# Optimization experiments

Hardware: AMD Instinct MI355X
Metric: run time of the kernel (lower is better)

## Reference

```python
import jax, jax.numpy as jnp
import numpy as np

B, S, H = 2, 2048, 1024
E, K, I = 8, 2, 512
NSH = 2
IS = I * NSH           # shared-expert intermediate = moe_inter * n_shared_experts
NUM_TASKS = 3
TEMP = 1.0             # router_temperature_init (eval: no annealing, no noise)


def setup_inputs() -> dict:
    key = jax.random.key(0)
    ks = jax.random.split(key, 11)
    s_h = 1.0 / np.sqrt(H).astype(np.float32)
    s_i = 1.0 / np.sqrt(I).astype(np.float32)
    s_is = 1.0 / np.sqrt(IS).astype(np.float32)
    return {
        "hidden_states": jax.random.normal(ks[0], (B, S, H), jnp.float32),
        "task_id": 1,
        "gate_w": jax.random.normal(ks[1], (E, H), jnp.float32) * s_h,
        "task_emb": jax.random.normal(ks[2], (NUM_TASKS, H), jnp.float32) * 0.02,
        "We_gate": jax.random.normal(ks[3], (E, H, I), jnp.float32) * s_h,
        "We_up": jax.random.normal(ks[4], (E, H, I), jnp.float32) * s_h,
        "We_down": jax.random.normal(ks[5], (E, I, H), jnp.float32) * s_i,
        "Ws_gate": jax.random.normal(ks[6], (H, IS), jnp.float32) * s_h,
        "Ws_up": jax.random.normal(ks[7], (H, IS), jnp.float32) * s_h,
        "Ws_down": jax.random.normal(ks[8], (IS, H), jnp.float32) * s_is,
        "Wc": jax.random.normal(ks[9], (H, 2), jnp.float32) * s_h,
    }


def _gelu(x):
    return jax.nn.gelu(x, approximate=False)  # matches torch F.gelu default (erf)


def reference(hidden_states, task_id, gate_w, task_emb, We_gate, We_up, We_down,
              Ws_gate, Ws_up, Ws_down, Wc):
    b, s, h = hidden_states.shape
    flat = hidden_states.reshape(-1, h)            # [T, H]
    T = flat.shape[0]

    # ---- NoisyTopKGating (eval: no gumbel noise, no dropout, no aux loss) ----
    gate_in = flat + task_emb[task_id]             # task-conditioned router input
    logits = (gate_in @ gate_w.T) / TEMP           # [T, E]
    scores = jax.nn.softmax(logits, axis=-1)
    topk_w, topk_idx = jax.lax.top_k(scores, K)    # [T, K]
    topk_w = topk_w / (topk_w.sum(-1, keepdims=True) + 1e-20)  # norm_topk_prob

    # dense combine weights [T, E]: zero except the top-k routed experts
    w_dense = jnp.zeros((T, E), scores.dtype).at[
        jnp.arange(T)[:, None], topk_idx].set(topk_w)

    # ---- routed experts: gated MLP per expert, weighted scatter-combine ----
    g = _gelu(jnp.einsum('td,edi->eti', flat, We_gate))   # [E, T, I]
    u = jnp.einsum('td,edi->eti', flat, We_up)            # [E, T, I]
    local = jnp.einsum('eti,te,eid->td', g * u, w_dense, We_down)
    local = local.reshape(b, s, h)

    # ---- shared expert (wider gated MLP over all tokens) ----
    shared = (_gelu(hidden_states @ Ws_gate) * (hidden_states @ Ws_up)) @ Ws_down

    # ---- combination gate: softmax over (local, shared) ----
    alpha = jax.nn.softmax(hidden_states @ Wc, axis=-1)   # [B, S, 2]
    return alpha[..., 0:1] * local + alpha[..., 1:2] * shared
```

## Files before the change

kernel.cpp:

```cpp
#include <hip/hip_runtime.h>
#include <hip/hip_bf16.h>


typedef short  s16x8 __attribute__((ext_vector_type(8)));
typedef __bf16 bf16x8 __attribute__((ext_vector_type(8)));
typedef float  f32x4 __attribute__((ext_vector_type(4)));

__device__ __forceinline__ float b2f(ushort u) {
  union { unsigned int i; float f; } v; v.i = ((unsigned int)u) << 16; return v.f;
}
__device__ __forceinline__ ushort f2b(float f) {
  union { float f; unsigned int i; } v; v.f = f;
  unsigned int r = v.i + 0x7fffu + ((v.i >> 16) & 1u);
  return (ushort)(r >> 16);
}
__device__ __forceinline__ f32x4 mfma_bf16(s16x8 a, s16x8 b, f32x4 c) {
  return __builtin_amdgcn_mfma_f32_16x16x32_bf16(
      __builtin_bit_cast(bf16x8, a), __builtin_bit_cast(bf16x8, b), c, 0, 0, 0);
}
__device__ __forceinline__ void gll16(const ushort* g, const ushort* l) {
  __builtin_amdgcn_global_load_lds(
      (const __attribute__((address_space(1))) unsigned int*)g,
      (__attribute__((address_space(3))) unsigned int*)l, 16, 0, 0);
}

__global__ __launch_bounds__(256) void transpose_all_k(
    const float* __restrict__ Weg, const float* __restrict__ Weu,
    const float* __restrict__ Wed, const float* __restrict__ Wsg,
    const float* __restrict__ Wsu, const float* __restrict__ Wsd,
    ushort* __restrict__ GT, ushort* __restrict__ UT, ushort* __restrict__ DT)
{
  const int z = blockIdx.z;
  const float* src; ushort* dst; int srcLd, dstLd, nx, ny;
  if (z < 8)       { src = Weg + (size_t)z * 512 * 1024;      dst = GT + (size_t)z * 512 * 1024; srcLd = 512;  dstLd = 1024; nx = 16; ny = 32; }
  else if (z < 16) { src = Weu + (size_t)(z - 8) * 512 * 1024; dst = UT + (size_t)(z - 8) * 512 * 1024; srcLd = 512; dstLd = 1024; nx = 16; ny = 32; }
  else if (z < 24) { src = Wed + (size_t)(z - 16) * 512 * 1024; dst = DT + (size_t)(z - 16) * 512; srcLd = 1024; dstLd = 5120; nx = 32; ny = 16; }
  else if (z == 24){ src = Wsg; dst = GT + 4096 * 1024; srcLd = 1024; dstLd = 1024; nx = 32; ny = 32; }
  else if (z == 25){ src = Wsu; dst = UT + 4096 * 1024; srcLd = 1024; dstLd = 1024; nx = 32; ny = 32; }
  else             { src = Wsd; dst = DT + 4096;        srcLd = 1024; dstLd = 5120; nx = 32; ny = 32; }
  if ((int)blockIdx.x >= nx || (int)blockIdx.y >= ny) return;

  __shared__ float tile[32][33];
  const int c0 = blockIdx.x * 32, r0 = blockIdx.y * 32;
  const int tx = threadIdx.x & 31, ty = threadIdx.x >> 5;
#pragma unroll
  for (int j = 0; j < 4; ++j)
    tile[ty + j * 8][tx] = src[(size_t)(r0 + ty + j * 8) * srcLd + c0 + tx];
  __syncthreads();
#pragma unroll
  for (int j = 0; j < 4; ++j)
    dst[(size_t)(c0 + ty + j * 8) * dstLd + r0 + tx] = f2b(tile[tx][ty + j * 8]);
}

__global__ __launch_bounds__(256) void router_k(
    const float* __restrict__ X, const float* __restrict__ Gw,
    const float* __restrict__ Temb, const int* __restrict__ task_id,
    const float* __restrict__ Wc, float* __restrict__ scales,
    int* __restrict__ topk, ushort* __restrict__ Xb)
{
  const int wid = threadIdx.x >> 6, lane = threadIdx.x & 63;
  const int t = blockIdx.x * 4 + wid;
  const float* xr = X + t * 1024;
  const float* er = Temb + task_id[0] * 1024;

  float x[16], xe[16];
#pragma unroll
  for (int c = 0; c < 4; ++c) {
    float4 v = *(const float4*)&xr[c * 256 + lane * 4];
    float4 e = *(const float4*)&er[c * 256 + lane * 4];
    x[c * 4 + 0] = v.x; x[c * 4 + 1] = v.y; x[c * 4 + 2] = v.z; x[c * 4 + 3] = v.w;
    xe[c * 4 + 0] = v.x + e.x; xe[c * 4 + 1] = v.y + e.y;
    xe[c * 4 + 2] = v.z + e.z; xe[c * 4 + 3] = v.w + e.w;
  }
#pragma unroll
  for (int c = 0; c < 4; ++c) {
    ushort4 o;
    o.x = f2b(x[c * 4 + 0]); o.y = f2b(x[c * 4 + 1]);
    o.z = f2b(x[c * 4 + 2]); o.w = f2b(x[c * 4 + 3]);
    *(ushort4*)&Xb[t * 1024 + c * 256 + lane * 4] = o;
  }
  float logit[8];
#pragma unroll
  for (int e = 0; e < 8; ++e) {
    float p = 0.f;
#pragma unroll
    for (int c = 0; c < 4; ++c) {
      float4 g = *(const float4*)&Gw[e * 1024 + c * 256 + lane * 4];
      p += xe[c * 4] * g.x + xe[c * 4 + 1] * g.y + xe[c * 4 + 2] * g.z + xe[c * 4 + 3] * g.w;
    }
#pragma unroll
    for (int off = 32; off; off >>= 1) p += __shfl_xor(p, off);
    logit[e] = p;
  }
  float m = logit[0];
#pragma unroll
  for (int e = 1; e < 8; ++e) m = fmaxf(m, logit[e]);
  float pr[8], s = 0.f;
#pragma unroll
  for (int e = 0; e < 8; ++e) { pr[e] = expf(logit[e] - m); s += pr[e]; }
  float inv = 1.f / s;
#pragma unroll
  for (int e = 0; e < 8; ++e) pr[e] *= inv;
  int i1 = 0; float m1 = pr[0];
#pragma unroll
  for (int e = 1; e < 8; ++e) if (pr[e] > m1) { m1 = pr[e]; i1 = e; }
  int i2 = -1; float m2 = -1.f;
#pragma unroll
  for (int e = 0; e < 8; ++e) if (e != i1 && pr[e] > m2) { m2 = pr[e]; i2 = e; }
  float dn = 1.f / (m1 + m2 + 1e-20f);
  float w1 = m1 * dn, w2 = m2 * dn;

  float a0 = 0.f, a1 = 0.f;
#pragma unroll
  for (int c = 0; c < 4; ++c)
#pragma unroll
    for (int j = 0; j < 4; ++j) {
      int h = c * 256 + lane * 4 + j;
      a0 += x[c * 4 + j] * Wc[h * 2];
      a1 += x[c * 4 + j] * Wc[h * 2 + 1];
    }
#pragma unroll
  for (int off = 32; off; off >>= 1) {
    a0 += __shfl_xor(a0, off); a1 += __shfl_xor(a1, off);
  }
  float am = fmaxf(a0, a1);
  float ea0 = expf(a0 - am), ea1 = expf(a1 - am);
  float al0 = ea0 / (ea0 + ea1), al1 = ea1 / (ea0 + ea1);

  if (lane == 0) {
    scales[t * 4 + 0] = al0 * w1;
    scales[t * 4 + 1] = al0 * w2;
    scales[t * 4 + 2] = al1;
    topk[t * 2 + 0] = i1;
    topk[t * 2 + 1] = i2;
  }
}

__global__ __launch_bounds__(256) void indexbuild_k(
    const int* __restrict__ topk, const float* __restrict__ scales,
    int* __restrict__ tokmap, int* __restrict__ tokrows,
    float* __restrict__ rowscale, int* __restrict__ meta)
{
  __shared__ int cnt[8], cnt2[8], base[8];
  const int tid = threadIdx.x;
  if (tid < 8) { cnt[tid] = 0; cnt2[tid] = 0; }
  __syncthreads();
  for (int t = tid; t < 4096; t += 256) {
    atomicAdd(&cnt[topk[t * 2]], 1);
    atomicAdd(&cnt[topk[t * 2 + 1]], 1);
  }
  __syncthreads();
  if (tid == 0) {
    int nb = 0;
    for (int e = 0; e < 8; ++e) {
      base[e] = nb * 128;
      int blocks = (cnt[e] + 127) >> 7;
      for (int j = 0; j < blocks; ++j) meta[nb + j] = e;
      nb += blocks;
    }
    meta[127] = nb;
  }
  __syncthreads();
  for (int t = tid; t < 4096; t += 256) {
#pragma unroll
    for (int r = 0; r < 2; ++r) {
      int e = topk[t * 2 + r];
      int slot = atomicAdd(&cnt2[e], 1);
      int row = base[e] + slot;
      tokmap[row] = t;
      rowscale[row] = scales[t * 4 + r];
      tokrows[t * 2 + r] = row;
    }
  }
  __syncthreads();
  for (int e = 0; e < 8; ++e) {
    int c = cnt[e], R = ((c + 127) >> 7) << 7;
    for (int j = c + tid; j < R; j += 256) {
      tokmap[base[e] + j] = 0;
      rowscale[base[e] + j] = 0.f;
    }
  }
}

__global__ __launch_bounds__(256) void gemm1_k(
    const ushort* __restrict__ Xb, const ushort* __restrict__ GT,
    const ushort* __restrict__ UT, const float* __restrict__ scales,
    const int* __restrict__ tokmap, const float* __restrict__ rowscale,
    const int* __restrict__ meta, ushort* __restrict__ Bg,
    ushort* __restrict__ Bs)
{
  __shared__ __align__(16) ushort lA[128 * 64];
  __shared__ __align__(16) ushort lG[64 * 64];
  __shared__ __align__(16) ushort lU[64 * 64];
  const int x = blockIdx.x, y = blockIdx.y;
  const bool routed = y < 72;
  if (routed && (x >= 8 || y >= meta[127])) return;

  const int tid = threadIdx.x, wid = tid >> 6, lane = tid & 63;
  const int col0 = x * 64;
  const int row0 = routed ? y * 128 : (y - 72) * 128;
  const int colG = routed ? (meta[y] * 512 + col0) : (4096 + col0);
  const int wr = (wid >> 1) * 64, wc = (wid & 1) * 32;
  ushort* __restrict__ Out = routed ? Bg : Bs;
  const int outLd = routed ? 512 : 1024;

  int aOff[4], gOff[2], ldsA[4], ldsG[2];
#pragma unroll
  for (int i = 0; i < 4; ++i) {
    int q = (i * 4 + wid) * 64 + lane;
    int r = q >> 3, c = q & 7, lc = c ^ (r & 7);
    int arow = routed ? tokmap[row0 + r] : (row0 + r);
    aOff[i] = arow * 1024 + lc * 8;
    ldsA[i] = (i * 4 + wid) * 512;
  }
#pragma unroll
  for (int i = 0; i < 2; ++i) {
    int q = (i * 4 + wid) * 64 + lane;
    int r = q >> 3, c = q & 7, lc = c ^ (r & 7);
    gOff[i] = (colG + r) * 1024 + lc * 8;
    ldsG[i] = (i * 4 + wid) * 512;
  }

  f32x4 accG[4][2] = {};
  f32x4 accU[4][2] = {};
  for (int k0 = 0; k0 < 1024; k0 += 64) {
    if (k0) __syncthreads();
#pragma unroll
    for (int i = 0; i < 4; ++i) gll16(Xb + aOff[i] + k0, lA + ldsA[i]);
#pragma unroll
    for (int i = 0; i < 2; ++i) gll16(GT + gOff[i] + k0, lG + ldsG[i]);
#pragma unroll
    for (int i = 0; i < 2; ++i) gll16(UT + gOff[i] + k0, lU + ldsG[i]);
    __syncthreads();
#pragma unroll
    for (int kc = 0; kc < 2; ++kc) {
      const int clog = kc * 4 + (lane >> 4);
      s16x8 af[4], gf[2], uf[2];
#pragma unroll
      for (int fr = 0; fr < 4; ++fr) {
        int rl = wr + fr * 16 + (lane & 15);
        af[fr] = *(const s16x8*)&lA[rl * 64 + ((clog ^ (rl & 7)) << 3)];
      }
#pragma unroll
      for (int cf = 0; cf < 2; ++cf) {
        int cl = wc + cf * 16 + (lane & 15);
        int off = cl * 64 + ((clog ^ (cl & 7)) << 3);
        gf[cf] = *(const s16x8*)&lG[off];
        uf[cf] = *(const s16x8*)&lU[off];
      }
#pragma unroll
      for (int fr = 0; fr < 4; ++fr)
#pragma unroll
        for (int cf = 0; cf < 2; ++cf) {
          accG[fr][cf] = mfma_bf16(af[fr], gf[cf], accG[fr][cf]);
          accU[fr][cf] = mfma_bf16(af[fr], uf[cf], accU[fr][cf]);
        }
    }
  }
#pragma unroll
  for (int fr = 0; fr < 4; ++fr)
#pragma unroll
    for (int r = 0; r < 4; ++r) {
      const int row = row0 + wr + fr * 16 + ((lane >> 4) << 2) + r;
      const float sc = routed ? rowscale[row] : scales[row * 4 + 2];
#pragma unroll
      for (int cf = 0; cf < 2; ++cf) {
        const int col = col0 + wc + cf * 16 + (lane & 15);
        float g = accG[fr][cf][r];
        float u = accU[fr][cf][r];
        float a = 0.5f * g * (1.0f + erff(g * 0.70710678118654752f));
        Out[(size_t)row * outLd + col] = f2b(a * u * sc);
      }
    }
}

template<int ROUTED>
__global__ __launch_bounds__(256) void gemm2_k(
    const ushort* __restrict__ A, const ushort* __restrict__ DT,
    const int* __restrict__ meta, const int* __restrict__ tokrows,
    const ushort* __restrict__ Rrows, ushort* __restrict__ OutB,
    float* __restrict__ OutF)
{
  __shared__ __align__(16) ushort lA[128 * 64];
  __shared__ __align__(16) ushort lB[128 * 64];
  int e = 0;
  if (ROUTED) {
    if ((int)blockIdx.y >= meta[127]) return;
    e = meta[blockIdx.y];
  }
  const int K = ROUTED ? 512 : 1024;
  const int bBase = ROUTED ? e * 512 : 4096;
  const int tid = threadIdx.x, wid = tid >> 6, lane = tid & 63;
  const int col0 = blockIdx.x * 128, row0 = blockIdx.y * 128;
  const int wr = (wid >> 1) * 64, wc = (wid & 1) * 64;

  int aOff[4], bOff[4], lds[4];
#pragma unroll
  for (int i = 0; i < 4; ++i) {
    int q = (i * 4 + wid) * 64 + lane;
    int r = q >> 3, c = q & 7, lc = c ^ (r & 7);
    aOff[i] = (row0 + r) * K + lc * 8;
    bOff[i] = (col0 + r) * 5120 + bBase + lc * 8;
    lds[i]  = (i * 4 + wid) * 512;
  }
  f32x4 acc[4][4] = {};
  for (int k0 = 0; k0 < K; k0 += 64) {
    if (k0) __syncthreads();
#pragma unroll
    for (int i = 0; i < 4; ++i) gll16(A + aOff[i] + k0, lA + lds[i]);
#pragma unroll
    for (int i = 0; i < 4; ++i) gll16(DT + bOff[i] + k0, lB + lds[i]);
    __syncthreads();
#pragma unroll
    for (int kc = 0; kc < 2; ++kc) {
      const int clog = kc * 4 + (lane >> 4);
      s16x8 af[4], bf[4];
#pragma unroll
      for (int fr = 0; fr < 4; ++fr) {
        int rl = wr + fr * 16 + (lane & 15);
        af[fr] = *(const s16x8*)&lA[rl * 64 + ((clog ^ (rl & 7)) << 3)];
      }
#pragma unroll
      for (int cf = 0; cf < 4; ++cf) {
        int cl = wc + cf * 16 + (lane & 15);
        bf[cf] = *(const s16x8*)&lB[cl * 64 + ((clog ^ (cl & 7)) << 3)];
      }
#pragma unroll
      for (int fr = 0; fr < 4; ++fr)
#pragma unroll
        for (int cf = 0; cf < 4; ++cf)
          acc[fr][cf] = mfma_bf16(af[fr], bf[cf], acc[fr][cf]);
    }
  }
#pragma unroll
  for (int fr = 0; fr < 4; ++fr)
#pragma unroll
    for (int r = 0; r < 4; ++r) {
      const int row = row0 + wr + fr * 16 + ((lane >> 4) << 2) + r;
      if (ROUTED) {
#pragma unroll
        for (int cf = 0; cf < 4; ++cf) {
          const int col = col0 + wc + cf * 16 + (lane & 15);
          OutB[row * 1024 + col] = f2b(acc[fr][cf][r]);
        }
      } else {
        const int r0 = tokrows[row * 2], r1 = tokrows[row * 2 + 1];
#pragma unroll
        for (int cf = 0; cf < 4; ++cf) {
          const int col = col0 + wc + cf * 16 + (lane & 15);
          float v = acc[fr][cf][r]
                  + b2f(Rrows[r0 * 1024 + col]) + b2f(Rrows[r1 * 1024 + col]);
          OutF[row * 1024 + col] = v;
        }
      }
    }
}

extern "C" void kernel_launch(void* const* d_in, const int* in_sizes, int n_in,
                              void* d_out, int out_size, void* d_ws, size_t ws_size,
                              hipStream_t stream) {
  const float* X    = (const float*)d_in[0];
  const int*   task = (const int*)  d_in[1];
  const float* Gw   = (const float*)d_in[2];
  const float* Temb = (const float*)d_in[3];
  const float* Weg  = (const float*)d_in[4];
  const float* Weu  = (const float*)d_in[5];
  const float* Wed  = (const float*)d_in[6];
  const float* Wsg  = (const float*)d_in[7];
  const float* Wsu  = (const float*)d_in[8];
  const float* Wsd  = (const float*)d_in[9];
  const float* Wc   = (const float*)d_in[10];

  char* ws = (char*)d_ws;
  float*  scales   = (float*)(ws + 0x00000);
  int*    topk     = (int*)  (ws + 0x10000);
  int*    tokmap   = (int*)  (ws + 0x18000);
  int*    tokrows  = (int*)  (ws + 0x22000);
  float*  rowscale = (float*)(ws + 0x2A000);
  int*    meta     = (int*)  (ws + 0x34000);
  ushort* Xb       = (ushort*)(ws + 0x40000);
  ushort* GT       = Xb + 4096 * 1024;
  ushort* UT       = GT + 5120 * 1024;
  ushort* DT       = UT + 5120 * 1024;
  ushort* Bg       = DT + 1024 * 5120;
  ushort* Bs       = Bg + 9216 * 512;
  ushort* out_r    = Bs + 4096 * 1024;

  transpose_all_k<<<dim3(32, 32, 27), 256, 0, stream>>>(
      Weg, Weu, Wed, Wsg, Wsu, Wsd, GT, UT, DT);

  router_k<<<1024, 256, 0, stream>>>(X, Gw, Temb, task, Wc, scales, topk, Xb);
  indexbuild_k<<<1, 256, 0, stream>>>(topk, scales, tokmap, tokrows, rowscale, meta);

  gemm1_k<<<dim3(16, 104), 256, 0, stream>>>(Xb, GT, UT, scales, tokmap, rowscale, meta, Bg, Bs);

  gemm2_k<1><<<dim3(8, 72), 256, 0, stream>>>(Bg, DT, meta, tokrows, (const ushort*)nullptr, out_r, (float*)nullptr);
  gemm2_k<0><<<dim3(8, 32), 256, 0, stream>>>(Bs, DT, meta, tokrows, out_r, (ushort*)nullptr, (float*)d_out);
}
```

Before: 176.7 us.

## Double-buffer LDS in both GEMM kernels and split transpose into exact grids

Both GEMM kernels move from a single LDS buffer to two ping-ponged buffers. The next K-tile is loaded with global_load_lds while the current one feeds the MFMAs, using explicit vmcnt waits and barriers, so load latency overlaps compute. The weight transpose is split into three launches whose grids match each matrix shape, which avoids launching blocks that exit at once. Doubling LDS use (64KB per block in gemm2) may lower occupancy, and the hand-written waitcnt counts must match the number of outstanding loads per stage.

```diff
diff --git a/kernel.cpp b/kernel.cpp
--- a/kernel.cpp
+++ b/kernel.cpp
@@ -24,22 +24,26 @@
       (__attribute__((address_space(3))) unsigned int*)l, 16, 0, 0);
 }
 
-__global__ __launch_bounds__(256) void transpose_all_k(
-    const float* __restrict__ Weg, const float* __restrict__ Weu,
-    const float* __restrict__ Wed, const float* __restrict__ Wsg,
-    const float* __restrict__ Wsu, const float* __restrict__ Wsd,
-    ushort* __restrict__ GT, ushort* __restrict__ UT, ushort* __restrict__ DT)
+template<int MODE>
+__global__ __launch_bounds__(256) void transpose_k(
+    const float* __restrict__ S0, const float* __restrict__ S1,
+    const float* __restrict__ S2, ushort* __restrict__ D0,
+    ushort* __restrict__ D1, ushort* __restrict__ D2)
 {
   const int z = blockIdx.z;
-  const float* src; ushort* dst; int srcLd, dstLd, nx, ny;
-  if (z < 8)       { src = Weg + (size_t)z * 512 * 1024;      dst = GT + (size_t)z * 512 * 1024; srcLd = 512;  dstLd = 1024; nx = 16; ny = 32; }
-  else if (z < 16) { src = Weu + (size_t)(z - 8) * 512 * 1024; dst = UT + (size_t)(z - 8) * 512 * 1024; srcLd = 512; dstLd = 1024; nx = 16; ny = 32; }
-  else if (z < 24) { src = Wed + (size_t)(z - 16) * 512 * 1024; dst = DT + (size_t)(z - 16) * 512; srcLd = 1024; dstLd = 5120; nx = 32; ny = 16; }
-  else if (z == 24){ src = Wsg; dst = GT + 4096 * 1024; srcLd = 1024; dstLd = 1024; nx = 32; ny = 32; }
-  else if (z == 25){ src = Wsu; dst = UT + 4096 * 1024; srcLd = 1024; dstLd = 1024; nx = 32; ny = 32; }
-  else             { src = Wsd; dst = DT + 4096;        srcLd = 1024; dstLd = 5120; nx = 32; ny = 32; }
-  if ((int)blockIdx.x >= nx || (int)blockIdx.y >= ny) return;
-
+  const float* src; ushort* dst; int srcLd, dstLd;
+  if (MODE == 0) {
+    src = (z < 8 ? S0 + (size_t)z * 512 * 1024 : S1 + (size_t)(z - 8) * 512 * 1024);
+    dst = (z < 8 ? D0 + (size_t)z * 512 * 1024 : D1 + (size_t)(z - 8) * 512 * 1024);
+    srcLd = 512; dstLd = 1024;
+  } else if (MODE == 1) {
+    src = S0 + (size_t)z * 512 * 1024; dst = D0 + (size_t)z * 512;
+    srcLd = 1024; dstLd = 5120;
+  } else {
+    src = (z == 0 ? S0 : z == 1 ? S1 : S2);
+    dst = (z == 0 ? D0 : z == 1 ? D1 : D2);
+    srcLd = 1024; dstLd = (z == 2 ? 5120 : 1024);
+  }
   __shared__ float tile[32][33];
   const int c0 = blockIdx.x * 32, r0 = blockIdx.y * 32;
   const int tx = threadIdx.x & 31, ty = threadIdx.x >> 5;
@@ -189,9 +193,9 @@
     const int* __restrict__ meta, ushort* __restrict__ Bg,
     ushort* __restrict__ Bs)
 {
-  __shared__ __align__(16) ushort lA[128 * 64];
-  __shared__ __align__(16) ushort lG[64 * 64];
-  __shared__ __align__(16) ushort lU[64 * 64];
+  __shared__ __align__(16) ushort lA[2][128 * 64];
+  __shared__ __align__(16) ushort lG[2][64 * 64];
+  __shared__ __align__(16) ushort lU[2][64 * 64];
   const int x = blockIdx.x, y = blockIdx.y;
   const bool routed = y < 72;
   if (routed && (x >= 8 || y >= meta[127])) return;
@@ -223,15 +227,16 @@
 
   f32x4 accG[4][2] = {};
   f32x4 accU[4][2] = {};
-  for (int k0 = 0; k0 < 1024; k0 += 64) {
-    if (k0) __syncthreads();
-#pragma unroll
-    for (int i = 0; i < 4; ++i) gll16(Xb + aOff[i] + k0, lA + ldsA[i]);
-#pragma unroll
-    for (int i = 0; i < 2; ++i) gll16(GT + gOff[i] + k0, lG + ldsG[i]);
-#pragma unroll
-    for (int i = 0; i < 2; ++i) gll16(UT + gOff[i] + k0, lU + ldsG[i]);
-    __syncthreads();
+
+  auto stage = [&](ushort* A_, ushort* G_, ushort* U_, int k0) {
+#pragma unroll
+    for (int i = 0; i < 4; ++i) gll16(Xb + aOff[i] + k0, A_ + ldsA[i]);
+#pragma unroll
+    for (int i = 0; i < 2; ++i) gll16(GT + gOff[i] + k0, G_ + ldsG[i]);
+#pragma unroll
+    for (int i = 0; i < 2; ++i) gll16(UT + gOff[i] + k0, U_ + ldsG[i]);
+  };
+  auto compute = [&](const ushort* A_, const ushort* G_, const ushort* U_) {
 #pragma unroll
     for (int kc = 0; kc < 2; ++kc) {
       const int clog = kc * 4 + (lane >> 4);
@@ -239,14 +244,14 @@
 #pragma unroll
       for (int fr = 0; fr < 4; ++fr) {
         int rl = wr + fr * 16 + (lane & 15);
-        af[fr] = *(const s16x8*)&lA[rl * 64 + ((clog ^ (rl & 7)) << 3)];
+        af[fr] = *(const s16x8*)&A_[rl * 64 + ((clog ^ (rl & 7)) << 3)];
       }
 #pragma unroll
       for (int cf = 0; cf < 2; ++cf) {
         int cl = wc + cf * 16 + (lane & 15);
         int off = cl * 64 + ((clog ^ (cl & 7)) << 3);
-        gf[cf] = *(const s16x8*)&lG[off];
-        uf[cf] = *(const s16x8*)&lU[off];
+        gf[cf] = *(const s16x8*)&G_[off];
+        uf[cf] = *(const s16x8*)&U_[off];
       }
 #pragma unroll
       for (int fr = 0; fr < 4; ++fr)
@@ -256,7 +261,28 @@
           accU[fr][cf] = mfma_bf16(af[fr], uf[cf], accU[fr][cf]);
         }
     }
-  }
+  };
+
+  stage(lA[0], lG[0], lU[0], 0);
+  for (int k0 = 0; k0 < 1024; k0 += 128) {
+    stage(lA[1], lG[1], lU[1], k0 + 64);
+    asm volatile("s_waitcnt vmcnt(8)" ::: "memory");
+    __builtin_amdgcn_s_barrier();
+    compute(lA[0], lG[0], lU[0]);
+    asm volatile("s_waitcnt lgkmcnt(0)" ::: "memory");
+    __builtin_amdgcn_s_barrier();
+    if (k0 + 128 < 1024) {
+      stage(lA[0], lG[0], lU[0], k0 + 128);
+      asm volatile("s_waitcnt vmcnt(8)" ::: "memory");
+    } else {
+      asm volatile("s_waitcnt vmcnt(0)" ::: "memory");
+    }
+    __builtin_amdgcn_s_barrier();
+    compute(lA[1], lG[1], lU[1]);
+    asm volatile("s_waitcnt lgkmcnt(0)" ::: "memory");
+    __builtin_amdgcn_s_barrier();
+  }
+
 #pragma unroll
   for (int fr = 0; fr < 4; ++fr)
 #pragma unroll
@@ -281,8 +307,8 @@
     const ushort* __restrict__ Rrows, ushort* __restrict__ OutB,
     float* __restrict__ OutF)
 {
-  __shared__ __align__(16) ushort lA[128 * 64];
-  __shared__ __align__(16) ushort lB[128 * 64];
+  __shared__ __align__(16) ushort lA[2][128 * 64];
+  __shared__ __align__(16) ushort lB[2][128 * 64];
   int e = 0;
   if (ROUTED) {
     if ((int)blockIdx.y >= meta[127]) return;
@@ -304,13 +330,14 @@
     lds[i]  = (i * 4 + wid) * 512;
   }
   f32x4 acc[4][4] = {};
-  for (int k0 = 0; k0 < K; k0 += 64) {
-    if (k0) __syncthreads();
-#pragma unroll
-    for (int i = 0; i < 4; ++i) gll16(A + aOff[i] + k0, lA + lds[i]);
-#pragma unroll
-    for (int i = 0; i < 4; ++i) gll16(DT + bOff[i] + k0, lB + lds[i]);
-    __syncthreads();
+
+  auto stage = [&](ushort* A_, ushort* B_, int k0) {
+#pragma unroll
+    for (int i = 0; i < 4; ++i) gll16(A + aOff[i] + k0, A_ + lds[i]);
+#pragma unroll
+    for (int i = 0; i < 4; ++i) gll16(DT + bOff[i] + k0, B_ + lds[i]);
+  };
+  auto compute = [&](const ushort* A_, const ushort* B_) {
 #pragma unroll
     for (int kc = 0; kc < 2; ++kc) {
       const int clog = kc * 4 + (lane >> 4);
@@ -318,12 +345,12 @@
 #pragma unroll
       for (int fr = 0; fr < 4; ++fr) {
         int rl = wr + fr * 16 + (lane & 15);
-        af[fr] = *(const s16x8*)&lA[rl * 64 + ((clog ^ (rl & 7)) << 3)];
+        af[fr] = *(const s16x8*)&A_[rl * 64 + ((clog ^ (rl & 7)) << 3)];
       }
 #pragma unroll
       for (int cf = 0; cf < 4; ++cf) {
         int cl = wc + cf * 16 + (lane & 15);
-        bf[cf] = *(const s16x8*)&lB[cl * 64 + ((clog ^ (cl & 7)) << 3)];
+        bf[cf] = *(const s16x8*)&B_[cl * 64 + ((clog ^ (cl & 7)) << 3)];
       }
 #pragma unroll
       for (int fr = 0; fr < 4; ++fr)
@@ -331,7 +358,28 @@
         for (int cf = 0; cf < 4; ++cf)
           acc[fr][cf] = mfma_bf16(af[fr], bf[cf], acc[fr][cf]);
     }
-  }
+  };
+
+  stage(lA[0], lB[0], 0);
+  for (int k0 = 0; k0 < K; k0 += 128) {
+    stage(lA[1], lB[1], k0 + 64);
+    asm volatile("s_waitcnt vmcnt(8)" ::: "memory");
+    __builtin_amdgcn_s_barrier();
+    compute(lA[0], lB[0]);
+    asm volatile("s_waitcnt lgkmcnt(0)" ::: "memory");
+    __builtin_amdgcn_s_barrier();
+    if (k0 + 128 < K) {
+      stage(lA[0], lB[0], k0 + 128);
+      asm volatile("s_waitcnt vmcnt(8)" ::: "memory");
+    } else {
+      asm volatile("s_waitcnt vmcnt(0)" ::: "memory");
+    }
+    __builtin_amdgcn_s_barrier();
+    compute(lA[1], lB[1]);
+    asm volatile("s_waitcnt lgkmcnt(0)" ::: "memory");
+    __builtin_amdgcn_s_barrier();
+  }
+
 #pragma unroll
   for (int fr = 0; fr < 4; ++fr)
 #pragma unroll
@@ -386,8 +434,10 @@
   ushort* Bs       = Bg + 9216 * 512;
   ushort* out_r    = Bs + 4096 * 1024;
 
-  transpose_all_k<<<dim3(32, 32, 27), 256, 0, stream>>>(
-      Weg, Weu, Wed, Wsg, Wsu, Wsd, GT, UT, DT);
+  transpose_k<0><<<dim3(16, 32, 16), 256, 0, stream>>>(Weg, Weu, nullptr, GT, UT, nullptr);
+  transpose_k<1><<<dim3(32, 16, 8), 256, 0, stream>>>(Wed, nullptr, nullptr, DT, nullptr, nullptr);
+  transpose_k<2><<<dim3(32, 32, 3), 256, 0, stream>>>(
+      Wsg, Wsu, Wsd, GT + 4096 * 1024, UT + 4096 * 1024, DT + 4096);
 
   router_k<<<1024, 256, 0, stream>>>(X, Gw, Temb, task, Wc, scales, topk, Xb);
   indexbuild_k<<<1, 256, 0, stream>>>(topk, scales, tokmap, tokrows, rowscale, meta);
```

Measured after the change: 181.9 us. 1.03x slower.

## Widen gemm1 tile to 128 columns and split weight transpose into exact-size launches

Applied to the files above, without the earlier changes.

gemm1 now computes a 128x128 output tile for both the gate and up projections per block instead of 128x64. This halves the number of blocks and the redundant re-reads of the gathered activation rows. In exchange, LDS use rises to 48KB per block and accumulator registers double, which may lower occupancy. The single transpose launch with many idle early-exit blocks is replaced by three launches sized to each weight group, and the global-to-LDS load indexing is rewritten to compute the same layout differently.

```diff
diff --git a/kernel.cpp b/kernel.cpp
--- a/kernel.cpp
+++ b/kernel.cpp
@@ -24,22 +24,26 @@
       (__attribute__((address_space(3))) unsigned int*)l, 16, 0, 0);
 }
 
-__global__ __launch_bounds__(256) void transpose_all_k(
-    const float* __restrict__ Weg, const float* __restrict__ Weu,
-    const float* __restrict__ Wed, const float* __restrict__ Wsg,
-    const float* __restrict__ Wsu, const float* __restrict__ Wsd,
-    ushort* __restrict__ GT, ushort* __restrict__ UT, ushort* __restrict__ DT)
+template<int MODE>
+__global__ __launch_bounds__(256) void transpose_k(
+    const float* __restrict__ S0, const float* __restrict__ S1,
+    const float* __restrict__ S2, ushort* __restrict__ D0,
+    ushort* __restrict__ D1, ushort* __restrict__ D2)
 {
   const int z = blockIdx.z;
-  const float* src; ushort* dst; int srcLd, dstLd, nx, ny;
-  if (z < 8)       { src = Weg + (size_t)z * 512 * 1024;      dst = GT + (size_t)z * 512 * 1024; srcLd = 512;  dstLd = 1024; nx = 16; ny = 32; }
-  else if (z < 16) { src = Weu + (size_t)(z - 8) * 512 * 1024; dst = UT + (size_t)(z - 8) * 512 * 1024; srcLd = 512; dstLd = 1024; nx = 16; ny = 32; }
-  else if (z < 24) { src = Wed + (size_t)(z - 16) * 512 * 1024; dst = DT + (size_t)(z - 16) * 512; srcLd = 1024; dstLd = 5120; nx = 32; ny = 16; }
-  else if (z == 24){ src = Wsg; dst = GT + 4096 * 1024; srcLd = 1024; dstLd = 1024; nx = 32; ny = 32; }
-  else if (z == 25){ src = Wsu; dst = UT + 4096 * 1024; srcLd = 1024; dstLd = 1024; nx = 32; ny = 32; }
-  else             { src = Wsd; dst = DT + 4096;        srcLd = 1024; dstLd = 5120; nx = 32; ny = 32; }
-  if ((int)blockIdx.x >= nx || (int)blockIdx.y >= ny) return;
-
+  const float* src; ushort* dst; int srcLd, dstLd;
+  if (MODE == 0) {
+    src = (z < 8 ? S0 + (size_t)z * 512 * 1024 : S1 + (size_t)(z - 8) * 512 * 1024);
+    dst = (z < 8 ? D0 + (size_t)z * 512 * 1024 : D1 + (size_t)(z - 8) * 512 * 1024);
+    srcLd = 512; dstLd = 1024;
+  } else if (MODE == 1) {
+    src = S0 + (size_t)z * 512 * 1024; dst = D0 + (size_t)z * 512;
+    srcLd = 1024; dstLd = 5120;
+  } else {
+    src = (z == 0 ? S0 : z == 1 ? S1 : S2);
+    dst = (z == 0 ? D0 : z == 1 ? D1 : D2);
+    srcLd = 1024; dstLd = (z == 2 ? 5120 : 1024);
+  }
   __shared__ float tile[32][33];
   const int c0 = blockIdx.x * 32, r0 = blockIdx.y * 32;
   const int tx = threadIdx.x & 31, ty = threadIdx.x >> 5;
@@ -190,59 +194,53 @@
     ushort* __restrict__ Bs)
 {
   __shared__ __align__(16) ushort lA[128 * 64];
-  __shared__ __align__(16) ushort lG[64 * 64];
-  __shared__ __align__(16) ushort lU[64 * 64];
+  __shared__ __align__(16) ushort lG[128 * 64];
+  __shared__ __align__(16) ushort lU[128 * 64];
   const int x = blockIdx.x, y = blockIdx.y;
   const bool routed = y < 72;
-  if (routed && (x >= 8 || y >= meta[127])) return;
+  if (routed && (x >= 4 || y >= meta[127])) return;
 
   const int tid = threadIdx.x, wid = tid >> 6, lane = tid & 63;
-  const int col0 = x * 64;
+  const int col0 = x * 128;
   const int row0 = routed ? y * 128 : (y - 72) * 128;
   const int colG = routed ? (meta[y] * 512 + col0) : (4096 + col0);
-  const int wr = (wid >> 1) * 64, wc = (wid & 1) * 32;
+  const int wr = (wid >> 1) * 64, wc = (wid & 1) * 64;
   ushort* __restrict__ Out = routed ? Bg : Bs;
   const int outLd = routed ? 512 : 1024;
 
-  int aOff[4], gOff[2], ldsA[4], ldsG[2];
+  int aOff[4], gOff[4], ldsO[4];
 #pragma unroll
   for (int i = 0; i < 4; ++i) {
-    int q = (i * 4 + wid) * 64 + lane;
+    int q = i * 256 + tid;
     int r = q >> 3, c = q & 7, lc = c ^ (r & 7);
     int arow = routed ? tokmap[row0 + r] : (row0 + r);
     aOff[i] = arow * 1024 + lc * 8;
-    ldsA[i] = (i * 4 + wid) * 512;
-  }
-#pragma unroll
-  for (int i = 0; i < 2; ++i) {
-    int q = (i * 4 + wid) * 64 + lane;
-    int r = q >> 3, c = q & 7, lc = c ^ (r & 7);
     gOff[i] = (colG + r) * 1024 + lc * 8;
-    ldsG[i] = (i * 4 + wid) * 512;
-  }
-
-  f32x4 accG[4][2] = {};
-  f32x4 accU[4][2] = {};
+    ldsO[i] = (i * 256 + (tid & ~63)) * 8;
+  }
+
+  f32x4 accG[4][4] = {};
+  f32x4 accU[4][4] = {};
   for (int k0 = 0; k0 < 1024; k0 += 64) {
     if (k0) __syncthreads();
 #pragma unroll
-    for (int i = 0; i < 4; ++i) gll16(Xb + aOff[i] + k0, lA + ldsA[i]);
-#pragma unroll
-    for (int i = 0; i < 2; ++i) gll16(GT + gOff[i] + k0, lG + ldsG[i]);
-#pragma unroll
-    for (int i = 0; i < 2; ++i) gll16(UT + gOff[i] + k0, lU + ldsG[i]);
+    for (int i = 0; i < 4; ++i) gll16(Xb + aOff[i] + k0, lA + ldsO[i] + lane * 8);
+#pragma unroll
+    for (int i = 0; i < 4; ++i) gll16(GT + gOff[i] + k0, lG + ldsO[i] + lane * 8);
+#pragma unroll
+    for (int i = 0; i < 4; ++i) gll16(UT + gOff[i] + k0, lU + ldsO[i] + lane * 8);
     __syncthreads();
 #pragma unroll
     for (int kc = 0; kc < 2; ++kc) {
       const int clog = kc * 4 + (lane >> 4);
-      s16x8 af[4], gf[2], uf[2];
+      s16x8 af[4], gf[4], uf[4];
 #pragma unroll
       for (int fr = 0; fr < 4; ++fr) {
         int rl = wr + fr * 16 + (lane & 15);
         af[fr] = *(const s16x8*)&lA[rl * 64 + ((clog ^ (rl & 7)) << 3)];
       }
 #pragma unroll
-      for (int cf = 0; cf < 2; ++cf) {
+      for (int cf = 0; cf < 4; ++cf) {
         int cl = wc + cf * 16 + (lane & 15);
         int off = cl * 64 + ((clog ^ (cl & 7)) << 3);
         gf[cf] = *(const s16x8*)&lG[off];
@@ -251,7 +249,7 @@
 #pragma unroll
       for (int fr = 0; fr < 4; ++fr)
 #pragma unroll
-        for (int cf = 0; cf < 2; ++cf) {
+        for (int cf = 0; cf < 4; ++cf) {
           accG[fr][cf] = mfma_bf16(af[fr], gf[cf], accG[fr][cf]);
           accU[fr][cf] = mfma_bf16(af[fr], uf[cf], accU[fr][cf]);
         }
@@ -264,7 +262,7 @@
       const int row = row0 + wr + fr * 16 + ((lane >> 4) << 2) + r;
       const float sc = routed ? rowscale[row] : scales[row * 4 + 2];
 #pragma unroll
-      for (int cf = 0; cf < 2; ++cf) {
+      for (int cf = 0; cf < 4; ++cf) {
         const int col = col0 + wc + cf * 16 + (lane & 15);
         float g = accG[fr][cf][r];
         float u = accU[fr][cf][r];
@@ -297,19 +295,19 @@
   int aOff[4], bOff[4], lds[4];
 #pragma unroll
   for (int i = 0; i < 4; ++i) {
-    int q = (i * 4 + wid) * 64 + lane;
+    int q = i * 256 + tid;
     int r = q >> 3, c = q & 7, lc = c ^ (r & 7);
     aOff[i] = (row0 + r) * K + lc * 8;
     bOff[i] = (col0 + r) * 5120 + bBase + lc * 8;
-    lds[i]  = (i * 4 + wid) * 512;
+    lds[i]  = (i * 256 + (tid & ~63)) * 8;
   }
   f32x4 acc[4][4] = {};
   for (int k0 = 0; k0 < K; k0 += 64) {
     if (k0) __syncthreads();
 #pragma unroll
-    for (int i = 0; i < 4; ++i) gll16(A + aOff[i] + k0, lA + lds[i]);
-#pragma unroll
-    for (int i = 0; i < 4; ++i) gll16(DT + bOff[i] + k0, lB + lds[i]);
+    for (int i = 0; i < 4; ++i) gll16(A + aOff[i] + k0, lA + lds[i] + lane * 8);
+#pragma unroll
+    for (int i = 0; i < 4; ++i) gll16(DT + bOff[i] + k0, lB + lds[i] + lane * 8);
     __syncthreads();
 #pragma unroll
     for (int kc = 0; kc < 2; ++kc) {
@@ -386,13 +384,15 @@
   ushort* Bs       = Bg + 9216 * 512;
   ushort* out_r    = Bs + 4096 * 1024;
 
-  transpose_all_k<<<dim3(32, 32, 27), 256, 0, stream>>>(
-      Weg, Weu, Wed, Wsg, Wsu, Wsd, GT, UT, DT);
+  transpose_k<0><<<dim3(16, 32, 16), 256, 0, stream>>>(Weg, Weu, nullptr, GT, UT, nullptr);
+  transpose_k<1><<<dim3(32, 16, 8), 256, 0, stream>>>(Wed, nullptr, nullptr, DT, nullptr, nullptr);
+  transpose_k<2><<<dim3(32, 32, 3), 256, 0, stream>>>(
+      Wsg, Wsu, Wsd, GT + 4096 * 1024, UT + 4096 * 1024, DT + 4096);
 
   router_k<<<1024, 256, 0, stream>>>(X, Gw, Temb, task, Wc, scales, topk, Xb);
   indexbuild_k<<<1, 256, 0, stream>>>(topk, scales, tokmap, tokrows, rowscale, meta);
 
-  gemm1_k<<<dim3(16, 104), 256, 0, stream>>>(Xb, GT, UT, scales, tokmap, rowscale, meta, Bg, Bs);
+  gemm1_k<<<dim3(8, 104), 256, 0, stream>>>(Xb, GT, UT, scales, tokmap, rowscale, meta, Bg, Bs);
 
   gemm2_k<1><<<dim3(8, 72), 256, 0, stream>>>(Bg, DT, meta, tokrows, (const ushort*)nullptr, out_r, (float*)nullptr);
   gemm2_k<0><<<dim3(8, 32), 256, 0, stream>>>(Bs, DT, meta, tokrows, out_r, (ushort*)nullptr, (float*)d_out);
```

After: 248.8 us. +40.9%, slower.
